# Kernel optimization log

Hardware: AMD Instinct MI355X
Metric: run time of the kernel (lower is better)

## Reference

```python
import jax, jax.numpy as jnp
import numpy as np

BN_EPS = 1e-5

def bn(x, gamma, beta):
    # x: [N, C]; BatchNorm2d over (batch, spatial) == node axis here (training-mode batch stats)
    mu = x.mean(axis=0, keepdims=True)
    var = x.var(axis=0, keepdims=True)
    return (x - mu) * jax.lax.rsqrt(var + BN_EPS) * gamma + beta

def octree_conv(x, neigh, W):
    # x: [N, Cin]; neigh: [N, K] with values in [0, N], N == empty neighbor
    # W: [K, Cin, Cout]. Sparse octree conv = neighbor gather + contraction.
    xp = jnp.concatenate([x, jnp.zeros((1, x.shape[1]), x.dtype)], axis=0)  # zero row for empties
    g = xp[neigh]                                  # [N, K, Cin]
    return jnp.einsum('nkc,kcd->nd', g, W)         # [N, Cout]

def setup_inputs() -> dict:
    key = jax.random.key(0)
    ks = jax.random.split(key, 8)
    N, Cin, Cout, Cb, K = 60000, 256, 512, 128, 27
    s = 0.05
    return {
        'x': jax.random.normal(ks[0], (1, Cin, N, 1), jnp.float32),
        'neigh': jax.random.randint(ks[1], (N, K), 0, N + 1),
        'W1a': jax.random.normal(ks[2], (Cb, Cin), jnp.float32) * s,
        'g1a': jnp.ones((Cb,), jnp.float32), 'b1a': jnp.zeros((Cb,), jnp.float32),
        'W3': jax.random.normal(ks[3], (K, Cb, Cb), jnp.float32) * s,
        'g3': jnp.ones((Cb,), jnp.float32), 'b3': jnp.zeros((Cb,), jnp.float32),
        'W1b': jax.random.normal(ks[4], (Cout, Cb), jnp.float32) * s,
        'g1b': jnp.ones((Cout,), jnp.float32), 'b1b': jnp.zeros((Cout,), jnp.float32),
        'Wc': jax.random.normal(ks[5], (Cout, Cin), jnp.float32) * s,
        'gc': jnp.ones((Cout,), jnp.float32), 'bc': jnp.zeros((Cout,), jnp.float32),
    }

def reference(x, neigh, W1a, g1a, b1a, W3, g3, b3, W1b, g1b, b1b, Wc, gc, bc):
    h = jnp.squeeze(x, axis=(0, 3)).T                         # [N, Cin]
    c1 = jax.nn.relu(bn(h @ W1a.T, g1a, b1a))                 # 1x1 conv + BN + ReLU -> [N, Cb]
    c2 = jax.nn.relu(bn(octree_conv(c1, neigh, W3), g3, b3))  # sparse 3x3 octree conv + BN + ReLU
    c3 = bn(c2 @ W1b.T, g1b, b1b)                             # 1x1 conv + BN -> [N, Cout]
    sc = bn(h @ Wc.T, gc, bc)                                 # shortcut 1x1 conv + BN (Cin != Cout)
    out = jax.nn.relu(c3 + sc)
    return out.T[None, :, :, None]                            # [1, Cout, N, 1]
```

## Files before the change

kernel.cpp:

```cpp
#include <hip/hip_runtime.h>


typedef __bf16 bf16x8 __attribute__((ext_vector_type(8)));
typedef float f32x4 __attribute__((ext_vector_type(4)));
typedef unsigned short u16x8 __attribute__((ext_vector_type(8)));
typedef unsigned short u16x4 __attribute__((ext_vector_type(4)));

__device__ __forceinline__ unsigned short f2bfu(float f) {
  union { float f; unsigned u; } v; v.f = f;
  unsigned r = v.u + 0x7fffu + ((v.u >> 16) & 1u);
  return (unsigned short)(r >> 16);
}
__device__ __forceinline__ float bfu2f(unsigned short s) {
  union { unsigned u; float f; } v; v.u = ((unsigned)s) << 16;
  return v.f;
}

__device__ __forceinline__ void gload_lds16(const unsigned short* g, unsigned short* l) {
  __builtin_amdgcn_global_load_lds(
      (const __attribute__((address_space(1))) unsigned int*)(unsigned long long)g,
      (__attribute__((address_space(3))) unsigned int*)(unsigned int)(unsigned long long)l,
      16, 0, 0);
}

__device__ __forceinline__ int xcd_swz(int bid, int nwg) {
  int q = nwg >> 3, r = nwg & 7;
  int xcd = bid & 7, idx = bid >> 3;
  int base = xcd < r ? xcd * (q + 1) : r * (q + 1) + (xcd - r) * q;
  return base + idx;
}

__global__ __launch_bounds__(256) void prep_weights(
    const float* __restrict__ W1a, const float* __restrict__ W3,
    const float* __restrict__ W1b, const float* __restrict__ Wc,
    unsigned short* __restrict__ w1a, unsigned short* __restrict__ w3t,
    unsigned short* __restrict__ w1b, unsigned short* __restrict__ wc) {
  int i = blockIdx.x * 256 + threadIdx.x;
  int stride = gridDim.x * 256;
  for (; i < 442368; i += stride) {
    if (i < 32768)  w1a[i] = f2bfu(W1a[i]);
    if (i < 65536)  w1b[i] = f2bfu(W1b[i]);
    if (i < 131072) wc[i]  = f2bfu(Wc[i]);
    int k = i >> 14, rr = i & 16383;
    int d = rr >> 7, c = rr & 127;
    w3t[i] = f2bfu(W3[(k << 14) + (c << 7) + d]);
  }
}

__global__ __launch_bounds__(256) void transpose_x(
    const float* __restrict__ x, unsigned short* __restrict__ h, int M) {
  __shared__ float tile[64][65];
  int n0 = blockIdx.x * 64, c0 = blockIdx.y * 64;
  int t = threadIdx.x;
  int nl = t & 63;
#pragma unroll
  for (int i = 0; i < 16; ++i) {
    int cl = i * 4 + (t >> 6);
    int n = n0 + nl;
    tile[cl][nl] = (n < M) ? x[(size_t)(c0 + cl) * M + n] : 0.f;
  }
  __syncthreads();
  int cl = t & 63;
#pragma unroll
  for (int i = 0; i < 16; ++i) {
    int nl2 = i * 4 + (t >> 6);
    int n = n0 + nl2;
    h[(size_t)n * 256 + c0 + cl] = f2bfu(tile[cl][nl2]);
  }
}

__global__ __launch_bounds__(512, 4) void gemm128(
    const unsigned short* __restrict__ A, const unsigned short* __restrict__ W,
    unsigned short* __restrict__ C, float* __restrict__ partials,
    int M, int Kd, int Nc, int ncol) {
  __shared__ unsigned short sA[2][128 * 64];
  __shared__ unsigned short sB[2][128 * 64];
  __shared__ float sStat[8][2][128];
  int t = threadIdx.x, wave = t >> 6, lane = t & 63;
  int flat = xcd_swz(blockIdx.x, gridDim.x);
  int n0 = (flat % ncol) * 128;
  int rowt = flat / ncol;
  int m0 = rowt * 128;
  int wr = wave >> 1, wcc = wave & 1;
  int l4 = lane >> 4, lc = lane & 15, lc7 = lc & 7;
  int lrow = lane >> 3, lch = lane & 7;
  f32x4 acc[2][4] = {};
  const int np = Kd >> 6;

  auto STAGE = [&](int p, int buf) {
    int k0 = p << 6;
#pragma unroll
    for (int i = 0; i < 2; ++i) {
      int row = wave * 16 + i * 8 + lrow;
      int sc = lch ^ (row & 7);
      gload_lds16(A + (size_t)(m0 + row) * Kd + k0 + sc * 8, &sA[buf][(wave * 16 + i * 8) * 64]);
    }
#pragma unroll
    for (int i = 0; i < 2; ++i) {
      int row = wave * 16 + i * 8 + lrow;
      int sc = lch ^ (row & 7);
      gload_lds16(W + (size_t)(n0 + row) * Kd + k0 + sc * 8, &sB[buf][(wave * 16 + i * 8) * 64]);
    }
  };
  auto COMPUTE = [&](int buf) {
#pragma unroll
    for (int kk = 0; kk < 2; ++kk) {
      bf16x8 af[2], bfr[4];
#pragma unroll
      for (int mi = 0; mi < 2; ++mi) {
        int row = wr * 32 + mi * 16 + lc;
        int chunk = (kk * 4 + l4) ^ lc7;
        af[mi] = __builtin_bit_cast(bf16x8, *(const u16x8*)(&sA[buf][row * 64 + chunk * 8]));
      }
#pragma unroll
      for (int ni = 0; ni < 4; ++ni) {
        int row = wcc * 64 + ni * 16 + lc;
        int chunk = (kk * 4 + l4) ^ lc7;
        bfr[ni] = __builtin_bit_cast(bf16x8, *(const u16x8*)(&sB[buf][row * 64 + chunk * 8]));
      }
      __builtin_amdgcn_s_setprio(1);
#pragma unroll
      for (int mi = 0; mi < 2; ++mi)
#pragma unroll
        for (int ni = 0; ni < 4; ++ni)
          acc[mi][ni] = __builtin_amdgcn_mfma_f32_16x16x32_bf16(af[mi], bfr[ni], acc[mi][ni], 0, 0, 0);
      __builtin_amdgcn_s_setprio(0);
    }
  };

  STAGE(0, 0);
  for (int p = 0; p < np; ++p) {
    int cur = p & 1;
    if (p < np - 1) {
      STAGE(p + 1, cur ^ 1);
      asm volatile("s_waitcnt vmcnt(4)" ::: "memory");
    } else {
      asm volatile("s_waitcnt vmcnt(0)" ::: "memory");
    }
    __builtin_amdgcn_sched_barrier(0);
    __builtin_amdgcn_s_barrier();
    __builtin_amdgcn_sched_barrier(0);
    COMPUTE(cur);
    __builtin_amdgcn_sched_barrier(0);
    __builtin_amdgcn_s_barrier();
  }

#pragma unroll
  for (int ni = 0; ni < 4; ++ni) {
    float s = 0.f, q = 0.f;
    int col = wcc * 64 + ni * 16 + lc;
#pragma unroll
    for (int mi = 0; mi < 2; ++mi)
#pragma unroll
      for (int j = 0; j < 4; ++j) {
        int n = m0 + wr * 32 + mi * 16 + l4 * 4 + j;
        unsigned short u = f2bfu(acc[mi][ni][j]);
        if (n < M) C[(size_t)n * Nc + n0 + col] = u;
        float v = bfu2f(u);
        s += v; q += v * v;
      }
    s += __shfl_xor(s, 16); s += __shfl_xor(s, 32);
    q += __shfl_xor(q, 16); q += __shfl_xor(q, 32);
    if (lane < 16) {
      sStat[wave][0][col] = s;
      sStat[wave][1][col] = q;
    }
  }
  __syncthreads();
  if (t < 128) {
    int wcs = t >> 6;
    float s = 0.f, q = 0.f;
#pragma unroll
    for (int g = 0; g < 4; ++g) {
      s += sStat[g * 2 + wcs][0][t];
      q += sStat[g * 2 + wcs][1][t];
    }
    partials[(size_t)rowt * (2 * Nc) + n0 + t] = s;
    partials[(size_t)rowt * (2 * Nc) + Nc + n0 + t] = q;
  }
}

__global__ __launch_bounds__(512, 4) void octree_gemm(
    const unsigned short* __restrict__ c1, const int* __restrict__ neigh,
    const unsigned short* __restrict__ w3t, unsigned short* __restrict__ c2p,
    float* __restrict__ partials, int M) {
  __shared__ unsigned short sA[2][128 * 64];
  __shared__ unsigned short sB[2][128 * 64];
  __shared__ union {
    unsigned short nidx[128 * 27];
    float stat[8][2][128];
  } u;
  int t = threadIdx.x, wave = t >> 6, lane = t & 63;
  int rowt = xcd_swz(blockIdx.x, gridDim.x);
  int m0 = rowt * 128;
  for (int i = t; i < 128 * 27; i += 512) {
    int row = i / 27;
    u.nidx[i] = (unsigned short)((m0 + row < M) ? neigh[(size_t)m0 * 27 + i] : M);
  }
  __syncthreads();

  int wr = wave >> 1, wcc = wave & 1;
  int l4 = lane >> 4, lc = lane & 15, lc7 = lc & 7;
  int lrow = lane >> 3, lch = lane & 7;
  f32x4 acc[2][4] = {};

  auto STAGE = [&](int p, int buf) {
    int k = p >> 1, c0 = (p & 1) << 6;
#pragma unroll
    for (int i = 0; i < 2; ++i) {
      int row = wave * 16 + i * 8 + lrow;
      int nr = u.nidx[row * 27 + k];
      int sc = lch ^ (row & 7);
      gload_lds16(c1 + ((size_t)nr << 7) + c0 + sc * 8, &sA[buf][(wave * 16 + i * 8) * 64]);
    }
    const unsigned short* wk = w3t + ((size_t)k << 14);
#pragma unroll
    for (int i = 0; i < 2; ++i) {
      int row = wave * 16 + i * 8 + lrow;
      int sc = lch ^ (row & 7);
      gload_lds16(wk + ((size_t)row << 7) + c0 + sc * 8, &sB[buf][(wave * 16 + i * 8) * 64]);
    }
  };
  auto COMPUTE = [&](int buf) {
#pragma unroll
    for (int kk = 0; kk < 2; ++kk) {
      bf16x8 af[2], bfr[4];
#pragma unroll
      for (int mi = 0; mi < 2; ++mi) {
        int row = wr * 32 + mi * 16 + lc;
        int chunk = (kk * 4 + l4) ^ lc7;
        af[mi] = __builtin_bit_cast(bf16x8, *(const u16x8*)(&sA[buf][row * 64 + chunk * 8]));
      }
#pragma unroll
      for (int ni = 0; ni < 4; ++ni) {
        int row = wcc * 64 + ni * 16 + lc;
        int chunk = (kk * 4 + l4) ^ lc7;
        bfr[ni] = __builtin_bit_cast(bf16x8, *(const u16x8*)(&sB[buf][row * 64 + chunk * 8]));
      }
      __builtin_amdgcn_s_setprio(1);
#pragma unroll
      for (int mi = 0; mi < 2; ++mi)
#pragma unroll
        for (int ni = 0; ni < 4; ++ni)
          acc[mi][ni] = __builtin_amdgcn_mfma_f32_16x16x32_bf16(af[mi], bfr[ni], acc[mi][ni], 0, 0, 0);
      __builtin_amdgcn_s_setprio(0);
    }
  };

  STAGE(0, 0);
  for (int p = 0; p < 54; ++p) {
    int cur = p & 1;
    if (p < 53) {
      STAGE(p + 1, cur ^ 1);
      asm volatile("s_waitcnt vmcnt(4)" ::: "memory");
    } else {
      asm volatile("s_waitcnt vmcnt(0)" ::: "memory");
    }
    __builtin_amdgcn_sched_barrier(0);
    __builtin_amdgcn_s_barrier();
    __builtin_amdgcn_sched_barrier(0);
    COMPUTE(cur);
    __builtin_amdgcn_sched_barrier(0);
    __builtin_amdgcn_s_barrier();
  }

#pragma unroll
  for (int ni = 0; ni < 4; ++ni) {
    float s = 0.f, q = 0.f;
    int col = wcc * 64 + ni * 16 + lc;
#pragma unroll
    for (int mi = 0; mi < 2; ++mi)
#pragma unroll
      for (int j = 0; j < 4; ++j) {
        int n = m0 + wr * 32 + mi * 16 + l4 * 4 + j;
        unsigned short uo = f2bfu(acc[mi][ni][j]);
        if (n < M) c2p[(size_t)n * 128 + col] = uo;
        float v = bfu2f(uo);
        s += v; q += v * v;
      }
    s += __shfl_xor(s, 16); s += __shfl_xor(s, 32);
    q += __shfl_xor(q, 16); q += __shfl_xor(q, 32);
    if (lane < 16) {
      u.stat[wave][0][col] = s;
      u.stat[wave][1][col] = q;
    }
  }
  __syncthreads();
  if (t < 128) {
    int wcs = t >> 6;
    float s = 0.f, q = 0.f;
#pragma unroll
    for (int g = 0; g < 4; ++g) {
      s += u.stat[g * 2 + wcs][0][t];
      q += u.stat[g * 2 + wcs][1][t];
    }
    partials[(size_t)rowt * 256 + t] = s;
    partials[(size_t)rowt * 256 + 128 + t] = q;
  }
}

__global__ __launch_bounds__(256) void bn_finalize(
    const float* __restrict__ partials, int nb, int C, int M,
    const float* __restrict__ g, const float* __restrict__ bt,
    float* __restrict__ ss) {
  int c = blockIdx.x;
  int t = threadIdx.x;
  float s = 0.f, s2 = 0.f;
  for (int b = t; b < nb; b += 256) {
    s += partials[(size_t)b * 2 * C + c];
    s2 += partials[(size_t)b * 2 * C + C + c];
  }
#pragma unroll
  for (int off = 32; off >= 1; off >>= 1) {
    s += __shfl_xor(s, off);
    s2 += __shfl_xor(s2, off);
  }
  __shared__ float sh[4][2];
  int wave = t >> 6, lane = t & 63;
  if (lane == 0) { sh[wave][0] = s; sh[wave][1] = s2; }
  __syncthreads();
  if (t == 0) {
    s = sh[0][0] + sh[1][0] + sh[2][0] + sh[3][0];
    s2 = sh[0][1] + sh[1][1] + sh[2][1] + sh[3][1];
    float mean = s / (float)M;
    float var = s2 / (float)M - mean * mean;
    float sc = g[c] * rsqrtf(var + 1e-5f);
    ss[c] = sc;
    ss[C + c] = bt[c] - mean * sc;
  }
}

__global__ __launch_bounds__(256) void bnrelu(
    const unsigned short* __restrict__ P, const float* __restrict__ ss,
    unsigned short* __restrict__ Aout, int total, int total2, int Cmask) {
  int i = (blockIdx.x * 256 + threadIdx.x) * 8;
  if (i >= total2) return;
  u16x8 o = {0, 0, 0, 0, 0, 0, 0, 0};
  if (i < total) {
    u16x8 v = *(const u16x8*)(P + i);
    int c0 = i & Cmask;
    int C = Cmask + 1;
#pragma unroll
    for (int j = 0; j < 8; ++j) {
      float f = bfu2f(v[j]) * ss[c0 + j] + ss[C + c0 + j];
      o[j] = f2bfu(fmaxf(f, 0.f));
    }
  }
  *(u16x8*)(Aout + i) = o;
}

__global__ __launch_bounds__(256) void final_out(
    const unsigned short* __restrict__ c3p, const unsigned short* __restrict__ scp,
    const float* __restrict__ ss3, const float* __restrict__ sssc,
    float* __restrict__ out, int M) {
  __shared__ float tile[64][129];
  int n0 = blockIdx.x * 64, c0 = blockIdx.y * 128;
  int t = threadIdx.x;
  int rowg = t >> 5, cg = (t & 31) * 4;
#pragma unroll
  for (int ps = 0; ps < 8; ++ps) {
    int nl = ps * 8 + rowg;
    int n = n0 + nl;
    float v0 = 0.f, v1 = 0.f, v2 = 0.f, v3 = 0.f;
    if (n < M) {
      u16x4 a = *(const u16x4*)(c3p + (size_t)n * 512 + c0 + cg);
      u16x4 b = *(const u16x4*)(scp + (size_t)n * 512 + c0 + cg);
      int c = c0 + cg;
      v0 = fmaxf(bfu2f(a[0]) * ss3[c + 0] + ss3[512 + c + 0] + bfu2f(b[0]) * sssc[c + 0] + sssc[512 + c + 0], 0.f);
      v1 = fmaxf(bfu2f(a[1]) * ss3[c + 1] + ss3[512 + c + 1] + bfu2f(b[1]) * sssc[c + 1] + sssc[512 + c + 1], 0.f);
      v2 = fmaxf(bfu2f(a[2]) * ss3[c + 2] + ss3[512 + c + 2] + bfu2f(b[2]) * sssc[c + 2] + sssc[512 + c + 2], 0.f);
      v3 = fmaxf(bfu2f(a[3]) * ss3[c + 3] + ss3[512 + c + 3] + bfu2f(b[3]) * sssc[c + 3] + sssc[512 + c + 3], 0.f);
    }
    tile[nl][cg + 0] = v0;
    tile[nl][cg + 1] = v1;
    tile[nl][cg + 2] = v2;
    tile[nl][cg + 3] = v3;
  }
  __syncthreads();
  int nl = t & 63, cq = t >> 6;
  int n = n0 + nl;
  if (n < M) {
#pragma unroll
    for (int i = 0; i < 32; ++i) {
      int cl = i * 4 + cq;
      out[(size_t)(c0 + cl) * M + n] = tile[nl][cl];
    }
  }
}

extern "C" void kernel_launch(void* const* d_in, const int* in_sizes, int n_in,
                              void* d_out, int out_size, void* d_ws, size_t ws_size,
                              hipStream_t stream) {
  const float* x   = (const float*)d_in[0];
  const int* neigh = (const int*)d_in[1];
  const float* W1a = (const float*)d_in[2];
  const float* g1a = (const float*)d_in[3];
  const float* b1a = (const float*)d_in[4];
  const float* W3  = (const float*)d_in[5];
  const float* g3  = (const float*)d_in[6];
  const float* b3  = (const float*)d_in[7];
  const float* W1b = (const float*)d_in[8];
  const float* g1b = (const float*)d_in[9];
  const float* b1b = (const float*)d_in[10];
  const float* Wc  = (const float*)d_in[11];
  const float* gc  = (const float*)d_in[12];
  const float* bc  = (const float*)d_in[13];
  float* out = (float*)d_out;

  const int M = in_sizes[1] / 27;
  const int MT = (M + 63) / 64;
  const int MTO = (M + 127) / 128;

  char* ws = (char*)d_ws;
  unsigned short* h   = (unsigned short*)(ws + 0);
  unsigned short* wA  = (unsigned short*)(ws + 30736384);
  unsigned short* wP  = (unsigned short*)(ws + 46104576);
  unsigned short* c3p = (unsigned short*)(ws + 61464576);
  unsigned short* scp = (unsigned short*)(ws + 122904576);
  unsigned short* w1a = (unsigned short*)(ws + 184344576);
  unsigned short* w3t = (unsigned short*)(ws + 184410112);
  unsigned short* w1b = (unsigned short*)(ws + 185294848);
  unsigned short* wc  = (unsigned short*)(ws + 185425920);
  float* ss1  = (float*)(ws + 185688064);
  float* ss2  = (float*)(ws + 185692160);
  float* ss3  = (float*)(ws + 185696256);
  float* sssc = (float*)(ws + 185700352);

  float* part12 = (float*)c3p;
  float* part3  = (float*)scp;
  float* partsc = (float*)wP;

  prep_weights<<<1728, 256, 0, stream>>>(W1a, W3, W1b, Wc, w1a, w3t, w1b, wc);
  transpose_x<<<dim3(MT, 4), 256, 0, stream>>>(x, h, M);

  const int total = M * 128, total2 = (MT * 64) * 128;
  const int bnGrid = (total2 / 8 + 255) / 256;

  gemm128<<<MTO, 512, 0, stream>>>(h, w1a, wP, part12, M, 256, 128, 1);
  bn_finalize<<<128, 256, 0, stream>>>(part12, MTO, 128, M, g1a, b1a, ss1);
  bnrelu<<<bnGrid, 256, 0, stream>>>(wP, ss1, wA, total, total2, 127);

  octree_gemm<<<MTO, 512, 0, stream>>>(wA, neigh, w3t, wP, part12, M);
  bn_finalize<<<128, 256, 0, stream>>>(part12, MTO, 128, M, g3, b3, ss2);
  bnrelu<<<bnGrid, 256, 0, stream>>>(wP, ss2, wA, total, total2, 127);

  gemm128<<<4 * MTO, 512, 0, stream>>>(wA, w1b, c3p, part3, M, 128, 512, 4);
  bn_finalize<<<512, 256, 0, stream>>>(part3, MTO, 512, M, g1b, b1b, ss3);

  gemm128<<<4 * MTO, 512, 0, stream>>>(h, wc, scp, partsc, M, 256, 512, 4);
  bn_finalize<<<512, 256, 0, stream>>>(partsc, MTO, 512, M, gc, bc, sssc);

  final_out<<<dim3(MT, 4), 256, 0, stream>>>(c3p, scp, ss3, sssc, out, M);
}
```

Before: 237.1 us.

## Co-schedule shortcut GEMM with octree conv and merge weight prep with transpose

Merges the weight-conversion and input-transpose kernels into one launch split by block index. The shortcut 1x1 GEMM (h @ Wc) now runs as extra blocks of the octree conv kernel, so the short shortcut tiles can fill the machine alongside the long gather-GEMM tiles instead of running as a separate launch. Partial-sum buffers are moved to distinct workspace regions so the concurrent outputs don't collide. This saves two launches and improves load balance, at the cost of larger, branchier kernels whose register and LDS budget is set by the heavier path.

New measurement: 225.6 us. 4.8% less time.

```diff
diff --git a/kernel.cpp b/kernel.cpp
--- a/kernel.cpp
+++ b/kernel.cpp
@@ -30,28 +30,29 @@
   return base + idx;
 }
 
-__global__ __launch_bounds__(256) void prep_weights(
+__global__ __launch_bounds__(256) void prep_transpose(
+    const float* __restrict__ x, unsigned short* __restrict__ h,
     const float* __restrict__ W1a, const float* __restrict__ W3,
     const float* __restrict__ W1b, const float* __restrict__ Wc,
     unsigned short* __restrict__ w1a, unsigned short* __restrict__ w3t,
-    unsigned short* __restrict__ w1b, unsigned short* __restrict__ wc) {
-  int i = blockIdx.x * 256 + threadIdx.x;
-  int stride = gridDim.x * 256;
-  for (; i < 442368; i += stride) {
-    if (i < 32768)  w1a[i] = f2bfu(W1a[i]);
-    if (i < 65536)  w1b[i] = f2bfu(W1b[i]);
-    if (i < 131072) wc[i]  = f2bfu(Wc[i]);
-    int k = i >> 14, rr = i & 16383;
-    int d = rr >> 7, c = rr & 127;
-    w3t[i] = f2bfu(W3[(k << 14) + (c << 7) + d]);
-  }
-}
-
-__global__ __launch_bounds__(256) void transpose_x(
-    const float* __restrict__ x, unsigned short* __restrict__ h, int M) {
+    unsigned short* __restrict__ w1b, unsigned short* __restrict__ wc,
+    int M, int MT) {
   __shared__ float tile[64][65];
-  int n0 = blockIdx.x * 64, c0 = blockIdx.y * 64;
   int t = threadIdx.x;
+  if (blockIdx.x < 432) {
+    int i = blockIdx.x * 256 + t;
+    for (; i < 442368; i += 432 * 256) {
+      if (i < 32768)  w1a[i] = f2bfu(W1a[i]);
+      if (i < 65536)  w1b[i] = f2bfu(W1b[i]);
+      if (i < 131072) wc[i]  = f2bfu(Wc[i]);
+      int k = i >> 14, rr = i & 16383;
+      int d = rr >> 7, c = rr & 127;
+      w3t[i] = f2bfu(W3[(k << 14) + (c << 7) + d]);
+    }
+    return;
+  }
+  int bid = blockIdx.x - 432;
+  int n0 = (bid % MT) * 64, c0 = (bid / MT) * 64;
   int nl = t & 63;
 #pragma unroll
   for (int i = 0; i < 16; ++i) {
@@ -180,10 +181,13 @@
   }
 }
 
-__global__ __launch_bounds__(512, 4) void octree_gemm(
+__global__ __launch_bounds__(512, 4) void octree_sc(
     const unsigned short* __restrict__ c1, const int* __restrict__ neigh,
     const unsigned short* __restrict__ w3t, unsigned short* __restrict__ c2p,
-    float* __restrict__ partials, int M) {
+    float* __restrict__ part12,
+    const unsigned short* __restrict__ h, const unsigned short* __restrict__ wc,
+    unsigned short* __restrict__ scp, float* __restrict__ partsc,
+    int M, int MTO) {
   __shared__ unsigned short sA[2][128 * 64];
   __shared__ unsigned short sB[2][128 * 64];
   __shared__ union {
@@ -191,111 +195,213 @@
     float stat[8][2][128];
   } u;
   int t = threadIdx.x, wave = t >> 6, lane = t & 63;
-  int rowt = xcd_swz(blockIdx.x, gridDim.x);
-  int m0 = rowt * 128;
-  for (int i = t; i < 128 * 27; i += 512) {
-    int row = i / 27;
-    u.nidx[i] = (unsigned short)((m0 + row < M) ? neigh[(size_t)m0 * 27 + i] : M);
-  }
-  __syncthreads();
-
   int wr = wave >> 1, wcc = wave & 1;
   int l4 = lane >> 4, lc = lane & 15, lc7 = lc & 7;
   int lrow = lane >> 3, lch = lane & 7;
   f32x4 acc[2][4] = {};
 
-  auto STAGE = [&](int p, int buf) {
-    int k = p >> 1, c0 = (p & 1) << 6;
-#pragma unroll
-    for (int i = 0; i < 2; ++i) {
-      int row = wave * 16 + i * 8 + lrow;
-      int nr = u.nidx[row * 27 + k];
-      int sc = lch ^ (row & 7);
-      gload_lds16(c1 + ((size_t)nr << 7) + c0 + sc * 8, &sA[buf][(wave * 16 + i * 8) * 64]);
-    }
-    const unsigned short* wk = w3t + ((size_t)k << 14);
-#pragma unroll
-    for (int i = 0; i < 2; ++i) {
-      int row = wave * 16 + i * 8 + lrow;
-      int sc = lch ^ (row & 7);
-      gload_lds16(wk + ((size_t)row << 7) + c0 + sc * 8, &sB[buf][(wave * 16 + i * 8) * 64]);
-    }
-  };
-  auto COMPUTE = [&](int buf) {
-#pragma unroll
-    for (int kk = 0; kk < 2; ++kk) {
-      bf16x8 af[2], bfr[4];
-#pragma unroll
-      for (int mi = 0; mi < 2; ++mi) {
-        int row = wr * 32 + mi * 16 + lc;
-        int chunk = (kk * 4 + l4) ^ lc7;
-        af[mi] = __builtin_bit_cast(bf16x8, *(const u16x8*)(&sA[buf][row * 64 + chunk * 8]));
-      }
-#pragma unroll
-      for (int ni = 0; ni < 4; ++ni) {
-        int row = wcc * 64 + ni * 16 + lc;
-        int chunk = (kk * 4 + l4) ^ lc7;
-        bfr[ni] = __builtin_bit_cast(bf16x8, *(const u16x8*)(&sB[buf][row * 64 + chunk * 8]));
-      }
-      __builtin_amdgcn_s_setprio(1);
+  if (blockIdx.x < (unsigned)MTO) {
+    int rowt = blockIdx.x;
+    int m0 = rowt * 128;
+    for (int i = t; i < 128 * 27; i += 512) {
+      int row = i / 27;
+      u.nidx[i] = (unsigned short)((m0 + row < M) ? neigh[(size_t)m0 * 27 + i] : M);
+    }
+    __syncthreads();
+
+    auto STAGE = [&](int p, int buf) {
+      int k = p >> 1, c0 = (p & 1) << 6;
+#pragma unroll
+      for (int i = 0; i < 2; ++i) {
+        int row = wave * 16 + i * 8 + lrow;
+        int nr = u.nidx[row * 27 + k];
+        int sc = lch ^ (row & 7);
+        gload_lds16(c1 + ((size_t)nr << 7) + c0 + sc * 8, &sA[buf][(wave * 16 + i * 8) * 64]);
+      }
+      const unsigned short* wk = w3t + ((size_t)k << 14);
+#pragma unroll
+      for (int i = 0; i < 2; ++i) {
+        int row = wave * 16 + i * 8 + lrow;
+        int sc = lch ^ (row & 7);
+        gload_lds16(wk + ((size_t)row << 7) + c0 + sc * 8, &sB[buf][(wave * 16 + i * 8) * 64]);
+      }
+    };
+    auto COMPUTE = [&](int buf) {
+#pragma unroll
+      for (int kk = 0; kk < 2; ++kk) {
+        bf16x8 af[2], bfr[4];
+#pragma unroll
+        for (int mi = 0; mi < 2; ++mi) {
+          int row = wr * 32 + mi * 16 + lc;
+          int chunk = (kk * 4 + l4) ^ lc7;
+          af[mi] = __builtin_bit_cast(bf16x8, *(const u16x8*)(&sA[buf][row * 64 + chunk * 8]));
+        }
+#pragma unroll
+        for (int ni = 0; ni < 4; ++ni) {
+          int row = wcc * 64 + ni * 16 + lc;
+          int chunk = (kk * 4 + l4) ^ lc7;
+          bfr[ni] = __builtin_bit_cast(bf16x8, *(const u16x8*)(&sB[buf][row * 64 + chunk * 8]));
+        }
+        __builtin_amdgcn_s_setprio(1);
+#pragma unroll
+        for (int mi = 0; mi < 2; ++mi)
+#pragma unroll
+          for (int ni = 0; ni < 4; ++ni)
+            acc[mi][ni] = __builtin_amdgcn_mfma_f32_16x16x32_bf16(af[mi], bfr[ni], acc[mi][ni], 0, 0, 0);
+        __builtin_amdgcn_s_setprio(0);
+      }
+    };
+
+    STAGE(0, 0);
+    for (int p = 0; p < 54; ++p) {
+      int cur = p & 1;
+      if (p < 53) {
+        STAGE(p + 1, cur ^ 1);
+        asm volatile("s_waitcnt vmcnt(4)" ::: "memory");
+      } else {
+        asm volatile("s_waitcnt vmcnt(0)" ::: "memory");
+      }
+      __builtin_amdgcn_sched_barrier(0);
+      __builtin_amdgcn_s_barrier();
+      __builtin_amdgcn_sched_barrier(0);
+      COMPUTE(cur);
+      __builtin_amdgcn_sched_barrier(0);
+      __builtin_amdgcn_s_barrier();
+    }
+
+#pragma unroll
+    for (int ni = 0; ni < 4; ++ni) {
+      float s = 0.f, q = 0.f;
+      int col = wcc * 64 + ni * 16 + lc;
 #pragma unroll
       for (int mi = 0; mi < 2; ++mi)
 #pragma unroll
-        for (int ni = 0; ni < 4; ++ni)
-          acc[mi][ni] = __builtin_amdgcn_mfma_f32_16x16x32_bf16(af[mi], bfr[ni], acc[mi][ni], 0, 0, 0);
-      __builtin_amdgcn_s_setprio(0);
-    }
-  };
-
-  STAGE(0, 0);
-  for (int p = 0; p < 54; ++p) {
-    int cur = p & 1;
-    if (p < 53) {
-      STAGE(p + 1, cur ^ 1);
-      asm volatile("s_waitcnt vmcnt(4)" ::: "memory");
-    } else {
-      asm volatile("s_waitcnt vmcnt(0)" ::: "memory");
-    }
-    __builtin_amdgcn_sched_barrier(0);
-    __builtin_amdgcn_s_barrier();
-    __builtin_amdgcn_sched_barrier(0);
-    COMPUTE(cur);
-    __builtin_amdgcn_sched_barrier(0);
-    __builtin_amdgcn_s_barrier();
-  }
-
-#pragma unroll
-  for (int ni = 0; ni < 4; ++ni) {
-    float s = 0.f, q = 0.f;
-    int col = wcc * 64 + ni * 16 + lc;
-#pragma unroll
-    for (int mi = 0; mi < 2; ++mi)
-#pragma unroll
-      for (int j = 0; j < 4; ++j) {
-        int n = m0 + wr * 32 + mi * 16 + l4 * 4 + j;
-        unsigned short uo = f2bfu(acc[mi][ni][j]);
-        if (n < M) c2p[(size_t)n * 128 + col] = uo;
-        float v = bfu2f(uo);
-        s += v; q += v * v;
-      }
-    s += __shfl_xor(s, 16); s += __shfl_xor(s, 32);
-    q += __shfl_xor(q, 16); q += __shfl_xor(q, 32);
-    if (lane < 16) {
-      u.stat[wave][0][col] = s;
-      u.stat[wave][1][col] = q;
-    }
-  }
-  __syncthreads();
-  if (t < 128) {
-    int wcs = t >> 6;
-    float s = 0.f, q = 0.f;
-#pragma unroll
-    for (int g = 0; g < 4; ++g) {
-      s += u.stat[g * 2 + wcs][0][t];
-      q += u.stat[g * 2 + wcs][1][t];
-    }
-    partials[(size_t)rowt * 256 + t] = s;
-    partials[(size_t)rowt * 256 + 128 + t] = q;
+        for (int j = 0; j < 4; ++j) {
+          int n = m0 + wr * 32 + mi * 16 + l4 * 4 + j;
+          unsigned short uo = f2bfu(acc[mi][ni][j]);
+          if (n < M) c2p[(size_t)n * 128 + col] = uo;
+          float v = bfu2f(uo);
+          s += v; q += v * v;
+        }
+      s += __shfl_xor(s, 16); s += __shfl_xor(s, 32);
+      q += __shfl_xor(q, 16); q += __shfl_xor(q, 32);
+      if (lane < 16) {
+        u.stat[wave][0][col] = s;
+        u.stat[wave][1][col] = q;
+      }
+    }
+    __syncthreads();
+    if (t < 128) {
+      int wcs = t >> 6;
+      float s = 0.f, q = 0.f;
+#pragma unroll
+      for (int g = 0; g < 4; ++g) {
+        s += u.stat[g * 2 + wcs][0][t];
+        q += u.stat[g * 2 + wcs][1][t];
+      }
+      part12[(size_t)rowt * 256 + t] = s;
+      part12[(size_t)rowt * 256 + 128 + t] = q;
+    }
+    return;
+  }
+
+  {
+    int flat = xcd_swz(blockIdx.x - MTO, gridDim.x - MTO);
+    int n0 = (flat & 3) * 128;
+    int rowt = flat >> 2;
+    int m0 = rowt * 128;
+
+    auto STAGE = [&](int p, int buf) {
+      int k0 = p << 6;
+#pragma unroll
+      for (int i = 0; i < 2; ++i) {
+        int row = wave * 16 + i * 8 + lrow;
+        int sc = lch ^ (row & 7);
+        gload_lds16(h + (size_t)(m0 + row) * 256 + k0 + sc * 8, &sA[buf][(wave * 16 + i * 8) * 64]);
+      }
+#pragma unroll
+      for (int i = 0; i < 2; ++i) {
+        int row = wave * 16 + i * 8 + lrow;
+        int sc = lch ^ (row & 7);
+        gload_lds16(wc + (size_t)(n0 + row) * 256 + k0 + sc * 8, &sB[buf][(wave * 16 + i * 8) * 64]);
+      }
+    };
+    auto COMPUTE = [&](int buf) {
+#pragma unroll
+      for (int kk = 0; kk < 2; ++kk) {
+        bf16x8 af[2], bfr[4];
+#pragma unroll
+        for (int mi = 0; mi < 2; ++mi) {
+          int row = wr * 32 + mi * 16 + lc;
+          int chunk = (kk * 4 + l4) ^ lc7;
+          af[mi] = __builtin_bit_cast(bf16x8, *(const u16x8*)(&sA[buf][row * 64 + chunk * 8]));
+        }
+#pragma unroll
+        for (int ni = 0; ni < 4; ++ni) {
+          int row = wcc * 64 + ni * 16 + lc;
+          int chunk = (kk * 4 + l4) ^ lc7;
+          bfr[ni] = __builtin_bit_cast(bf16x8, *(const u16x8*)(&sB[buf][row * 64 + chunk * 8]));
+        }
+        __builtin_amdgcn_s_setprio(1);
+#pragma unroll
+        for (int mi = 0; mi < 2; ++mi)
+#pragma unroll
+          for (int ni = 0; ni < 4; ++ni)
+            acc[mi][ni] = __builtin_amdgcn_mfma_f32_16x16x32_bf16(af[mi], bfr[ni], acc[mi][ni], 0, 0, 0);
+        __builtin_amdgcn_s_setprio(0);
+      }
+    };
+
+    STAGE(0, 0);
+    for (int p = 0; p < 4; ++p) {
+      int cur = p & 1;
+      if (p < 3) {
+        STAGE(p + 1, cur ^ 1);
+        asm volatile("s_waitcnt vmcnt(4)" ::: "memory");
+      } else {
+        asm volatile("s_waitcnt vmcnt(0)" ::: "memory");
+      }
+      __builtin_amdgcn_sched_barrier(0);
+      __builtin_amdgcn_s_barrier();
+      __builtin_amdgcn_sched_barrier(0);
+      COMPUTE(cur);
+      __builtin_amdgcn_sched_barrier(0);
+      __builtin_amdgcn_s_barrier();
+    }
+
+#pragma unroll
+    for (int ni = 0; ni < 4; ++ni) {
+      float s = 0.f, q = 0.f;
+      int col = wcc * 64 + ni * 16 + lc;
+#pragma unroll
+      for (int mi = 0; mi < 2; ++mi)
+#pragma unroll
+        for (int j = 0; j < 4; ++j) {
+          int n = m0 + wr * 32 + mi * 16 + l4 * 4 + j;
+          unsigned short uo = f2bfu(acc[mi][ni][j]);
+          if (n < M) scp[(size_t)n * 512 + n0 + col] = uo;
+          float v = bfu2f(uo);
+          s += v; q += v * v;
+        }
+      s += __shfl_xor(s, 16); s += __shfl_xor(s, 32);
+      q += __shfl_xor(q, 16); q += __shfl_xor(q, 32);
+      if (lane < 16) {
+        u.stat[wave][0][col] = s;
+        u.stat[wave][1][col] = q;
+      }
+    }
+    __syncthreads();
+    if (t < 128) {
+      int wcs = t >> 6;
+      float s = 0.f, q = 0.f;
+#pragma unroll
+      for (int g = 0; g < 4; ++g) {
+        s += u.stat[g * 2 + wcs][0][t];
+        q += u.stat[g * 2 + wcs][1][t];
+      }
+      partsc[(size_t)rowt * 1024 + n0 + t] = s;
+      partsc[(size_t)rowt * 1024 + 512 + n0 + t] = q;
+    }
   }
 }
 
@@ -426,29 +532,29 @@
   float* ss3  = (float*)(ws + 185696256);
   float* sssc = (float*)(ws + 185700352);
 
-  float* part12 = (float*)c3p;
-  float* part3  = (float*)scp;
-  float* partsc = (float*)wP;
-
-  prep_weights<<<1728, 256, 0, stream>>>(W1a, W3, W1b, Wc, w1a, w3t, w1b, wc);
-  transpose_x<<<dim3(MT, 4), 256, 0, stream>>>(x, h, M);
+  float* part1  = (float*)(ws + 61464576);
+  float* part12 = (float*)(ws + 61464576 + 1048576);
+  float* partsc = (float*)(ws + 61464576 + 2097152);
+  float* part3  = (float*)wP;
+
+  prep_transpose<<<432 + MT * 4, 256, 0, stream>>>(
+      x, h, W1a, W3, W1b, Wc, w1a, w3t, w1b, wc, M, MT);
 
   const int total = M * 128, total2 = (MT * 64) * 128;
   const int bnGrid = (total2 / 8 + 255) / 256;
 
-  gemm128<<<MTO, 512, 0, stream>>>(h, w1a, wP, part12, M, 256, 128, 1);
-  bn_finalize<<<128, 256, 0, stream>>>(part12, MTO, 128, M, g1a, b1a, ss1);
+  gemm128<<<MTO, 512, 0, stream>>>(h, w1a, wP, part1, M, 256, 128, 1);
+  bn_finalize<<<128, 256, 0, stream>>>(part1, MTO, 128, M, g1a, b1a, ss1);
   bnrelu<<<bnGrid, 256, 0, stream>>>(wP, ss1, wA, total, total2, 127);
 
-  octree_gemm<<<MTO, 512, 0, stream>>>(wA, neigh, w3t, wP, part12, M);
+  octree_sc<<<MTO + 4 * MTO, 512, 0, stream>>>(
+      wA, neigh, w3t, wP, part12, h, wc, scp, partsc, M, MTO);
   bn_finalize<<<128, 256, 0, stream>>>(part12, MTO, 128, M, g3, b3, ss2);
+  bn_finalize<<<512, 256, 0, stream>>>(partsc, MTO, 512, M, gc, bc, sssc);
   bnrelu<<<bnGrid, 256, 0, stream>>>(wP, ss2, wA, total, total2, 127);
 
   gemm128<<<4 * MTO, 512, 0, stream>>>(wA, w1b, c3p, part3, M, 128, 512, 4);
   bn_finalize<<<512, 256, 0, stream>>>(part3, MTO, 512, M, g1b, b1b, ss3);
 
-  gemm128<<<4 * MTO, 512, 0, stream>>>(h, wc, scp, partsc, M, 256, 512, 4);
-  bn_finalize<<<512, 256, 0, stream>>>(partsc, MTO, 512, M, gc, bc, sssc);
-
   final_out<<<dim3(MT, 4), 256, 0, stream>>>(c3p, scp, ss3, sssc, out, M);
 }
```
